# Kernel optimization log

Hardware: AMD Instinct MI355X
Metric: run time of the kernel (lower is better)

The kernel has to match this reference:

```python
import jax, jax.numpy as jnp
import numpy as np

N = 65536      # total nodes
B = 128        # graphs per batch
NPG = N // B   # nodes per graph (equal-size graphs)
IN = 128       # in_channels
H = 128        # hidden_channels
E = 1048576    # spatial edges
K = 8          # kNN neighbors
L = 3          # num_layers
EPS = 1e-5     # GraphNorm eps
SLOPE = 0.01   # leaky_relu default negative_slope


def setup_inputs() -> dict:
    key = jax.random.key(0)
    ks = jax.random.split(key, 16)
    x = jax.random.normal(ks[0], (N, IN), jnp.float32)
    edge_index = jax.random.randint(ks[1], (2, E), 0, N, dtype=jnp.int32)
    batch = jnp.repeat(jnp.arange(B, dtype=jnp.int32), NPG)
    s = 0.05
    inp = {
        'x': x, 'edge_index': edge_index, 'batch': batch,
        'emb_w': jax.random.normal(ks[2], (IN, H), jnp.float32) * s,
        'emb_b': jax.random.normal(ks[3], (H,), jnp.float32) * s,
        'conv_w': jax.random.normal(ks[4], (L - 1, H, H), jnp.float32) * s,
        'conv_b': jax.random.normal(ks[5], (L - 1, H), jnp.float32) * s,
        'fconv_w': jax.random.normal(ks[6], (L - 1, H, H), jnp.float32) * s,
        'fconv_b': jax.random.normal(ks[7], (L - 1, H), jnp.float32) * s,
        'norm_w': 1.0 + jax.random.normal(ks[8], (L - 1, H), jnp.float32) * s,
        'norm_b': jax.random.normal(ks[9], (L - 1, H), jnp.float32) * s,
        'norm_ms': 1.0 + jax.random.normal(ks[10], (L - 1, H), jnp.float32) * s,
        'fnorm_w': 1.0 + jax.random.normal(ks[11], (L - 1, H), jnp.float32) * s,
        'fnorm_b': jax.random.normal(ks[12], (L - 1, H), jnp.float32) * s,
        'fnorm_ms': 1.0 + jax.random.normal(ks[13], (L - 1, H), jnp.float32) * s,
    }
    return inp


def _segment_mean(v, seg, num):
    s = jax.ops.segment_sum(v, seg, num_segments=num)
    c = jax.ops.segment_sum(jnp.ones((v.shape[0], 1), v.dtype), seg, num_segments=num)
    return s / jnp.maximum(c, 1.0)


def _gcn_conv(h, src, dst, W, b):
    # GCNConv: h @ W, add self-loops, symmetric normalization, scatter-add.
    hw = h @ W
    deg = jax.ops.segment_sum(jnp.ones(src.shape[0], hw.dtype), dst, num_segments=N) + 1.0
    dinv = jax.lax.rsqrt(deg)
    msgs = (dinv[src] * dinv[dst])[:, None] * hw[src]
    agg = jnp.zeros_like(hw).at[dst].add(msgs)
    agg = agg + (dinv * dinv)[:, None] * hw  # self-loop contribution
    return agg + b


def _graph_norm(v, batch, w, bsh, ms):
    mean = _segment_mean(v, batch, B)                  # [B,H]
    out = v - mean[batch] * ms
    var = _segment_mean(out * out, batch, B)
    std = jnp.sqrt(var + EPS)
    return w * out / std[batch] + bsh


def _knn_graph_cosine(h):
    # per-graph cosine kNN (loop=False); equal-size graphs -> blocked [B,n,n] sim
    hb = h.reshape(B, NPG, H)
    nrm = jnp.linalg.norm(hb, axis=-1, keepdims=True)
    hn = hb / jnp.maximum(nrm, 1e-12)
    sim = jnp.einsum('bnd,bmd->bnm', hn, hn)
    sim = sim - 2.0 * jnp.eye(NPG, dtype=sim.dtype)    # exclude self-loops
    _, idx = jax.lax.top_k(sim, K)                     # [B,NPG,K] in-graph ids
    offs = (jnp.arange(B, dtype=idx.dtype) * NPG)[:, None, None]
    src = (idx + offs).reshape(-1).astype(jnp.int32)   # neighbors (sources)
    dst = jnp.repeat(jnp.arange(N, dtype=jnp.int32), K)
    return src, dst


def reference(x, edge_index, batch, emb_w, emb_b, conv_w, conv_b, fconv_w, fconv_b,
              norm_w, norm_b, norm_ms, fnorm_w, fnorm_b, fnorm_ms):
    h = x @ emb_w + emb_b
    fsrc, fdst = _knn_graph_cosine(h)
    src, dst = edge_index[0], edge_index[1]
    all_h = []
    for i in range(L - 1):
        h1 = _gcn_conv(h, src, dst, conv_w[i], conv_b[i])
        h1 = _graph_norm(h1, batch, norm_w[i], norm_b[i], norm_ms[i])
        h1 = jax.nn.leaky_relu(h1, SLOPE)              # dropout is identity (eval)
        f = _gcn_conv(h1, fsrc, fdst, fconv_w[i], fconv_b[i])
        f = _graph_norm(f, batch, fnorm_w[i], fnorm_b[i], fnorm_ms[i])
        f = jax.nn.leaky_relu(f, SLOPE)
        h = (h1 + f) * 0.5
        all_h.append(h)
    # faithful to original: indexes all_x[i-1] for i in range(num_layers)
    gf = jnp.zeros((B, H), h.dtype)
    for i in range(L):
        gf = gf + _segment_mean(all_h[i - 1], batch, B)
    return gf
```

## Files before the change

### kernel.cpp

```cpp
#include <hip/hip_runtime.h>

typedef unsigned short u16;
typedef unsigned int   u32;
typedef unsigned char  u8;
typedef __bf16 bf16x8 __attribute__((ext_vector_type(8)));
typedef unsigned short us8 __attribute__((ext_vector_type(8)));
typedef float f32x4 __attribute__((ext_vector_type(4)));

#define NN 65536
#define EE 1048576
#define NPGC 512
#define BGR 128
#define EMAX 32
#define NB 128
#define BSLOT 96
#define EBSLOT 10240
#define FP8S 32.0f
#define FP8SI (1.0f/32.0f)

__device__ inline float bf2f(u16 b){ u32 u=((u32)b)<<16; float f; __builtin_memcpy(&f,&u,4); return f; }
__device__ inline u16 f2bf(float f){ u32 u; __builtin_memcpy(&u,&f,4); u32 r=(u+0x7FFFu+((u>>16)&1u))>>16; return (u16)r; }
__device__ inline u8 f2fp8(float f){
  int p = __builtin_amdgcn_cvt_pk_fp8_f32(f, f, 0, false);
  return (u8)(p & 0xFF);
}

struct PTab { const void* src[9]; int off[9]; };
__global__ __launch_bounds__(256) void prep_params(const float* __restrict__ emb_w,
    const float* __restrict__ conv_w, const float* __restrict__ fconv_w, u16* __restrict__ pwt,
    PTab tab, u16* __restrict__ pw)
{
  int i = blockIdx.x*256 + threadIdx.x;
  if (i < 5*16384) {
    int m = i >> 14, j = i & 16383;
    int n = j >> 7, k = j & 127;
    const float* src = (m == 0) ? emb_w : (m <= 2) ? conv_w + (m-1)*16384 : fconv_w + (m-3)*16384;
    pwt[i] = f2bf(src[k*128 + n]);
  } else {
    int s = i - 5*16384;
    if (s < 2176) {
      int t = 0;
      #pragma unroll
      for (int k = 1; k < 9; k++) if (s >= tab.off[k]) t = k;
      pw[s] = f2bf(((const float*)tab.src[t])[s - tab.off[t]]);
    }
  }
}

__global__ __launch_bounds__(256) void bucket_edges(const int* __restrict__ srcp,
    const int* __restrict__ dstp, int* __restrict__ boff, u32* __restrict__ ebuf)
{
  __shared__ u32 buf[NB][BSLOT];
  __shared__ int cnt[NB], gbase[NB];
  const int tid = threadIdx.x;
  for (int b = tid; b < NB; b += 256) cnt[b] = 0;
  __syncthreads();
  const int base = blockIdx.x * 4096;
  #pragma unroll
  for (int v = 0; v < 4; v++) {
    const int e = base + (v*256 + tid)*4;
    int4 dv = *reinterpret_cast<const int4*>(dstp + e);
    int4 sv = *reinterpret_cast<const int4*>(srcp + e);
    #pragma unroll
    for (int t = 0; t < 4; t++) {
      u32 d = ((u32)((&dv.x)[t])) & (NN-1);
      u32 s = ((u32)((&sv.x)[t])) & (NN-1);
      int b = d >> 9;
      int p = atomicAdd(&cnt[b], 1);
      if (p < BSLOT) buf[b][p] = (d << 16) | s;
    }
  }
  __syncthreads();
  for (int b = tid; b < NB; b += 256) gbase[b] = atomicAdd(&boff[b], min(cnt[b], BSLOT));
  __syncthreads();
  const int wave = tid >> 6, lane = tid & 63;
  for (int b = wave; b < NB; b += 4) {
    const int c = min(cnt[b], BSLOT);
    const int gb = gbase[b];
    for (int i = lane; i < c; i += 64) {
      int gi = gb + i;
      if (gi < EBSLOT) ebuf[(size_t)b*EBSLOT + gi] = buf[b][i];
    }
  }
}

__global__ __launch_bounds__(256) void fill_ell(const int* __restrict__ boff,
    const u32* __restrict__ ebuf, int* __restrict__ pos, u16* __restrict__ elln)
{
  __shared__ u16 lell[512*EMAX];
  __shared__ int lcnt[512];
  const int b = blockIdx.x;
  const int tid = threadIdx.x;
  for (int i = tid; i < 512; i += 256) lcnt[i] = 0;
  __syncthreads();
  const int cnt = min(boff[b], EBSLOT);
  const u32* eb = ebuf + (size_t)b*EBSLOT;
  for (int i = tid; i < cnt; i += 256) {
    u32 v = eb[i];
    int dl = (v >> 16) & 511;
    int p = atomicAdd(&lcnt[dl], 1);
    if (p < EMAX) lell[dl*EMAX + p] = (u16)(v & 0xFFFFu);
  }
  __syncthreads();
  const int nbase = b * 512;
  for (int i = tid; i < 512; i += 256) pos[nbase + i] = lcnt[i];
  u32* dst = reinterpret_cast<u32*>(elln + ((size_t)nbase << 5));
  const u32* src = reinterpret_cast<const u32*>(lell);
  for (int i = tid; i < 512*16; i += 256) dst[i] = src[i];
}

__global__ __launch_bounds__(256) void gemm_emb_bt(const float* __restrict__ X,
    const u16* __restrict__ BtE, const u16* __restrict__ bias, const u16* __restrict__ BtC,
    const int* __restrict__ pos, u16* __restrict__ Ch, float* __restrict__ rinv,
    u8* __restrict__ Chw)
{
  __shared__ __align__(16) u16 hs[64][136];
  const int tid = threadIdx.x;
  const int wave = tid >> 6, lane = tid & 63, q = lane >> 4, l15 = lane & 15;
  const long arow = (long)blockIdx.x*64 + wave*16 + l15;
  const float* Ap = X + arow*128;
  f32x4 acc[8] = {};
  #pragma unroll
  for (int ks = 0; ks < 4; ks++) {
    const int k0 = ks*32 + q*8;
    float4 u0 = *reinterpret_cast<const float4*>(Ap + k0);
    float4 u1 = *reinterpret_cast<const float4*>(Ap + k0 + 4);
    us8 a;
    a[0]=f2bf(u0.x); a[1]=f2bf(u0.y); a[2]=f2bf(u0.z); a[3]=f2bf(u0.w);
    a[4]=f2bf(u1.x); a[5]=f2bf(u1.y); a[6]=f2bf(u1.z); a[7]=f2bf(u1.w);
    bf16x8 af = __builtin_bit_cast(bf16x8, a);
    #pragma unroll
    for (int nt = 0; nt < 8; nt++) {
      bf16x8 bf = __builtin_bit_cast(bf16x8,
          *reinterpret_cast<const us8*>(BtE + (nt*16 + l15)*128 + k0));
      acc[nt] = __builtin_amdgcn_mfma_f32_16x16x32_bf16(af, bf, acc[nt], 0, 0, 0);
    }
  }
  const long orow0 = (long)blockIdx.x*64 + wave*16 + q*4;
  float bvt[8];
  #pragma unroll
  for (int nt = 0; nt < 8; nt++) bvt[nt] = bf2f(bias[nt*16 + l15]);
  #pragma unroll
  for (int r = 0; r < 4; r++) {
    float ss = 0.f;
    const int lrow = wave*16 + q*4 + r;
    #pragma unroll
    for (int nt = 0; nt < 8; nt++) {
      float hv = acc[nt][r] + bvt[nt];
      u16 hb = f2bf(hv);
      Ch[(orow0 + r)*128 + nt*16 + l15] = hb;
      hs[lrow][nt*16 + l15] = hb;
      ss += hv*hv;
    }
    #pragma unroll
    for (int m = 1; m < 16; m <<= 1) ss += __shfl_xor(ss, m, 64);
    if (l15 == 0) rinv[orow0 + r] = 1.0f / fmaxf(sqrtf(ss), 1e-12f);
  }
  f32x4 acc2[8] = {};
  #pragma unroll
  for (int ks = 0; ks < 4; ks++) {
    const int k0 = ks*32 + q*8;
    bf16x8 af = __builtin_bit_cast(bf16x8,
        *reinterpret_cast<const us8*>(&hs[wave*16 + l15][k0]));
    #pragma unroll
    for (int nt = 0; nt < 8; nt++) {
      bf16x8 bf = __builtin_bit_cast(bf16x8,
          *reinterpret_cast<const us8*>(BtC + (nt*16 + l15)*128 + k0));
      acc2[nt] = __builtin_amdgcn_mfma_f32_16x16x32_bf16(af, bf, acc2[nt], 0, 0, 0);
    }
  }
  float scl[4];
  #pragma unroll
  for (int r = 0; r < 4; r++) scl[r] = rsqrtf((float)pos[orow0 + r] + 1.0f) * FP8S;
  #pragma unroll
  for (int nt = 0; nt < 8; nt++) {
    int col = nt*16 + l15;
    #pragma unroll
    for (int r = 0; r < 4; r++)
      Chw[(orow0 + r)*128 + col] = f2fp8(acc2[nt][r] * scl[r]);
  }
}

__global__ __launch_bounds__(256) void gemm_norm(const u16* __restrict__ h1raw,
    const u16* __restrict__ Bt, const float* __restrict__ ssum, const float* __restrict__ ssq,
    const u16* __restrict__ gw, const u16* __restrict__ gb, const u16* __restrict__ gms,
    u16* __restrict__ h1norm, u16* __restrict__ C)
{
  __shared__ float As[4][128], Bs[4][128];
  const int tid = threadIdx.x;
  const int gidx = blockIdx.x >> 3;
  const int wave = tid >> 6, lane = tid & 63, q = lane >> 4, l15 = lane & 15;
  #pragma unroll
  for (int cc = 0; cc < 2; cc++) {
    int c = cc*64 + lane;
    float mean = ssum[gidx*128 + c] * (1.0f/512.0f);
    float e2   = ssq [gidx*128 + c] * (1.0f/512.0f);
    float sub  = mean * bf2f(gms[c]);
    float var  = e2 - 2.0f*sub*mean + sub*sub;
    float istd = rsqrtf(var + 1e-5f);
    float A = istd * bf2f(gw[c]);
    As[wave][c] = A;
    Bs[wave][c] = bf2f(gb[c]) - sub*A;
  }
  const long arow = (long)blockIdx.x*64 + wave*16 + l15;
  const u16* Ap = h1raw + arow*128;
  f32x4 acc[8] = {};
  #pragma unroll
  for (int ks = 0; ks < 4; ks++) {
    const int k0 = ks*32 + q*8;
    us8 raw = *reinterpret_cast<const us8*>(Ap + k0);
    us8 af;
    #pragma unroll
    for (int j = 0; j < 8; j++) {
      float o = As[wave][k0+j] * bf2f(raw[j]) + Bs[wave][k0+j];
      o = (o >= 0.f) ? o : 0.01f * o;
      af[j] = f2bf(o);
    }
    *reinterpret_cast<us8*>(h1norm + arow*128 + k0) = af;
    bf16x8 afv = __builtin_bit_cast(bf16x8, af);
    #pragma unroll
    for (int nt = 0; nt < 8; nt++) {
      bf16x8 bf = __builtin_bit_cast(bf16x8,
          *reinterpret_cast<const us8*>(Bt + (nt*16 + l15)*128 + k0));
      acc[nt] = __builtin_amdgcn_mfma_f32_16x16x32_bf16(afv, bf, acc[nt], 0, 0, 0);
    }
  }
  const long orow0 = (long)blockIdx.x*64 + wave*16 + q*4;
  #pragma unroll
  for (int nt = 0; nt < 8; nt++) {
    int col = nt*16 + l15;
    #pragma unroll
    for (int r = 0; r < 4; r++)
      C[(orow0 + r)*128 + col] = f2bf(acc[nt][r]);
  }
}

__global__ __launch_bounds__(256) void gn_apply_gemm(const u16* __restrict__ fraw,
    const u16* __restrict__ h1n, const u16* __restrict__ Bt,
    const float* __restrict__ ssum, const float* __restrict__ ssq,
    const u16* __restrict__ gw, const u16* __restrict__ gb, const u16* __restrict__ gms,
    const int* __restrict__ pos, float* __restrict__ gf, u8* __restrict__ C)
{
  __shared__ float As[4][128], Bs[4][128];
  __shared__ float gpart[4][128];
  const int tid = threadIdx.x;
  const int gidx = blockIdx.x >> 3;
  const int wave = tid >> 6, lane = tid & 63, q = lane >> 4, l15 = lane & 15;
  #pragma unroll
  for (int cc = 0; cc < 2; cc++) {
    int c = cc*64 + lane;
    float mean = ssum[gidx*128 + c] * (1.0f/512.0f);
    float e2   = ssq [gidx*128 + c] * (1.0f/512.0f);
    float sub  = mean * bf2f(gms[c]);
    float var  = e2 - 2.0f*sub*mean + sub*sub;
    float istd = rsqrtf(var + 1e-5f);
    float A = istd * bf2f(gw[c]);
    As[wave][c] = A;
    Bs[wave][c] = bf2f(gb[c]) - sub*A;
  }
  const long arow = (long)blockIdx.x*64 + wave*16 + l15;
  const u16* Fp = fraw + arow*128;
  const u16* Hp = h1n  + arow*128;
  f32x4 acc[8] = {};
  float hv[4][8];
  #pragma unroll
  for (int ks = 0; ks < 4; ks++) {
    const int k0 = ks*32 + q*8;
    us8 fr = *reinterpret_cast<const us8*>(Fp + k0);
    us8 hr = *reinterpret_cast<const us8*>(Hp + k0);
    us8 af;
    #pragma unroll
    for (int j = 0; j < 8; j++) {
      float o = As[wave][k0+j] * bf2f(fr[j]) + Bs[wave][k0+j];
      o = (o >= 0.f) ? o : 0.01f * o;
      float h = 0.5f * (bf2f(hr[j]) + o);
      hv[ks][j] = h;
      af[j] = f2bf(h);
    }
    bf16x8 afv = __builtin_bit_cast(bf16x8, af);
    #pragma unroll
    for (int nt = 0; nt < 8; nt++) {
      bf16x8 bf = __builtin_bit_cast(bf16x8,
          *reinterpret_cast<const us8*>(Bt + (nt*16 + l15)*128 + k0));
      acc[nt] = __builtin_amdgcn_mfma_f32_16x16x32_bf16(afv, bf, acc[nt], 0, 0, 0);
    }
  }
  const long orow0 = (long)blockIdx.x*64 + wave*16 + q*4;
  float scl[4];
  #pragma unroll
  for (int r = 0; r < 4; r++) scl[r] = rsqrtf((float)pos[orow0 + r] + 1.0f) * FP8S;
  #pragma unroll
  for (int nt = 0; nt < 8; nt++) {
    int col = nt*16 + l15;
    #pragma unroll
    for (int r = 0; r < 4; r++)
      C[(orow0 + r)*128 + col] = f2fp8(acc[nt][r] * scl[r]);
  }
  #pragma unroll
  for (int ks = 0; ks < 4; ks++) {
    #pragma unroll
    for (int j = 0; j < 8; j++) {
      float v = hv[ks][j];
      v += __shfl_xor(v, 1, 64);
      v += __shfl_xor(v, 2, 64);
      v += __shfl_xor(v, 4, 64);
      v += __shfl_xor(v, 8, 64);
      if (l15 == 0) gpart[wave][ks*32 + q*8 + j] = v;
    }
  }
  __syncthreads();
  if (tid < 128) {
    float s = gpart[0][tid] + gpart[1][tid] + gpart[2][tid] + gpart[3][tid];
    atomicAdd(&gf[gidx*128 + tid], s * (1.0f/512.0f));
  }
}

__device__ inline u32 mkkey(float v, u32 col){
  u32 b; __builtin_memcpy(&b, &v, 4);
  b ^= (u32)(((int)b >> 31)) | 0x80000000u;
  return (b & 0xFFFFFE00u) | col;
}
#define TOP8_INS(tv, key) { \
  tv[0] = max(tv[0], (key)); \
  u32 lo_, hi_; \
  lo_ = min(tv[0],tv[1]); hi_ = max(tv[0],tv[1]); tv[0]=lo_; tv[1]=hi_; \
  lo_ = min(tv[1],tv[2]); hi_ = max(tv[1],tv[2]); tv[1]=lo_; tv[2]=hi_; \
  lo_ = min(tv[2],tv[3]); hi_ = max(tv[2],tv[3]); tv[2]=lo_; tv[3]=hi_; \
  lo_ = min(tv[3],tv[4]); hi_ = max(tv[3],tv[4]); tv[3]=lo_; tv[4]=hi_; \
  lo_ = min(tv[4],tv[5]); hi_ = max(tv[4],tv[5]); tv[4]=lo_; tv[5]=hi_; \
  lo_ = min(tv[5],tv[6]); hi_ = max(tv[5],tv[6]); tv[5]=lo_; tv[6]=hi_; \
  lo_ = min(tv[6],tv[7]); hi_ = max(tv[6],tv[7]); tv[6]=lo_; tv[7]=hi_; }

__global__ __launch_bounds__(256, 4) void knn_topk(const u16* __restrict__ h,
    const float* __restrict__ rinv, int* __restrict__ fsrc)
{
  __shared__ __align__(16) u16 Bb[64*136];
  __shared__ __align__(16) u32 simb[64*68];
  __shared__ float rb[64];
  const int tid = threadIdx.x;
  const int g = blockIdx.x & 127, tile = blockIdx.x >> 7;
  const int gbase = g * NPGC;
  const int abase = gbase + tile * 64;
  const int wave = tid >> 6, lane = tid & 63, q = lane >> 4, l15 = lane & 15;

  us8 afr[4];
  #pragma unroll
  for (int ks = 0; ks < 4; ks++)
    afr[ks] = *reinterpret_cast<const us8*>(h + (size_t)(abase + wave*16 + l15)*128 + ks*32 + q*8);

  const int r0 = tid >> 4, c80 = (tid & 15) * 8;
  us8 breg[4];
  #pragma unroll
  for (int it = 0; it < 4; it++)
    breg[it] = *reinterpret_cast<const us8*>(h + (size_t)(gbase + r0 + it*16)*128 + c80);
  float rbreg = (tid < 64) ? rinv[gbase + tid] : 0.f;

  const int srow = tid >> 2, ssub = tid & 3;
  u32 tv[8];
  #pragma unroll
  for (int t = 0; t < 8; t++) tv[t] = 0u;

  for (int ch = 0; ch < 8; ch++) {
    #pragma unroll
    for (int it = 0; it < 4; it++)
      *reinterpret_cast<us8*>(&Bb[(r0 + it*16)*136 + c80]) = breg[it];
    if (tid < 64) rb[tid] = rbreg;
    __syncthreads();
    if (ch < 7) {
      #pragma unroll
      for (int it = 0; it < 4; it++)
        breg[it] = *reinterpret_cast<const us8*>(h + (size_t)(gbase + (ch+1)*64 + r0 + it*16)*128 + c80);
      if (tid < 64) rbreg = rinv[gbase + (ch+1)*64 + tid];
    }
    f32x4 acc[4] = {};
    #pragma unroll
    for (int ks = 0; ks < 4; ks++) {
      int k0 = ks*32 + q*8;
      bf16x8 af = __builtin_bit_cast(bf16x8, afr[ks]);
      #pragma unroll
      for (int ct = 0; ct < 4; ct++) {
        bf16x8 bf = __builtin_bit_cast(bf16x8, *reinterpret_cast<const us8*>(&Bb[(ct*16 + l15)*136 + k0]));
        acc[ct] = __builtin_amdgcn_mfma_f32_16x16x32_bf16(af, bf, acc[ct], 0, 0, 0);
      }
    }
    #pragma unroll
    for (int ct = 0; ct < 4; ct++) {
      int lc = ct*16 + l15;
      float rbv = rb[lc];
      #pragma unroll
      for (int r = 0; r < 4; r++) {
        int lr = wave*16 + q*4 + r;
        u32 key = mkkey(acc[ct][r] * rbv, (u32)(ch*64 + lc));
        if (tile*64 + lr == ch*64 + lc) key = 0u;
        simb[lr*68 + lc] = key;
      }
    }
    __syncthreads();
    const u32* sp = &simb[srow*68 + ssub*16];
    #pragma unroll
    for (int u = 0; u < 4; u++) {
      uint4 kv = *reinterpret_cast<const uint4*>(sp + 4*u);
      TOP8_INS(tv, kv.x); TOP8_INS(tv, kv.y); TOP8_INS(tv, kv.z); TOP8_INS(tv, kv.w);
    }
    __syncthreads();
  }
  u32* candk = simb;
  #pragma unroll
  for (int t = 0; t < 8; t++) candk[srow*33 + ssub*8 + t] = tv[t];
  __syncthreads();
  if (tid < 64) {
    u32 bv[8];
    #pragma unroll
    for (int t = 0; t < 8; t++) bv[t] = 0u;
    for (int t = 0; t < 32; t++) {
      u32 key = candk[tid*33 + t];
      TOP8_INS(bv, key);
    }
    size_t node = abase + tid;
    #pragma unroll
    for (int k2 = 0; k2 < 8; k2++) fsrc[node*8 + k2] = gbase + (int)(bv[k2] & 511u);
  }
}

__device__ inline void acc4(u32 vv, bool on, float& a0, float& a1, float& a2, float& a3){
  float c0 = __builtin_amdgcn_cvt_f32_fp8((int)vv, 0);
  float c1 = __builtin_amdgcn_cvt_f32_fp8((int)vv, 1);
  float c2 = __builtin_amdgcn_cvt_f32_fp8((int)vv, 2);
  float c3 = __builtin_amdgcn_cvt_f32_fp8((int)vv, 3);
  a0 += on ? c0 : 0.f; a1 += on ? c1 : 0.f;
  a2 += on ? c2 : 0.f; a3 += on ? c3 : 0.f;
}
__global__ __launch_bounds__(256) void agg_spatial(const u32* __restrict__ hw32,
    const u16* __restrict__ elln, const int* __restrict__ pos,
    const u16* __restrict__ bias, u16* __restrict__ outp,
    float* __restrict__ ssum, float* __restrict__ ssq)
{
  __shared__ f32x4 sred[4][64], qred[4][64];
  const int g = blockIdx.x & 127, sub = blockIdx.x >> 7;
  const int wave = threadIdx.x >> 6, lane = threadIdx.x & 63;
  const int half = lane >> 5, cl = lane & 31;
  const int nbase = g*NPGC + sub*32 + wave*8;
  float bv[4];
  #pragma unroll
  for (int k = 0; k < 4; k++) bv[k] = bf2f(bias[4*cl + k]);
  float sa0=0,sa1=0,sa2=0,sa3=0, qa0=0,qa1=0,qa2=0,qa3=0;
  for (int t = 0; t < 4; t++) {
    const int node = nbase + 2*t + half;
    const u16* row = elln + ((size_t)node << 5);
    const int tot = pos[node];
    const int d = min(tot, EMAX);
    const int dmax = max(d, __shfl_xor(d, 32, 64));
    const float dnS = rsqrtf((float)tot + 1.0f) * FP8SI;
    const u32 sv = hw32[(size_t)node*32 + cl];
    float a0=0,a1=0,a2=0,a3=0;
    if (dmax > 0) {
      us8 iv0 = *reinterpret_cast<const us8*>(row);
      us8 iv1 = *reinterpret_cast<const us8*>(row + 8);
      u32 v[16];
      #pragma unroll
      for (int u = 0; u < 8; u++) v[u] = hw32[(size_t)iv0[u]*32 + cl];
      const bool two = (dmax > 8);
      if (two) {
        #pragma unroll
        for (int u = 0; u < 8; u++) v[8+u] = hw32[(size_t)iv1[u]*32 + cl];
      }
      #pragma unroll
      for (int u = 0; u < 8; u++) acc4(v[u], u < d, a0, a1, a2, a3);
      if (two) {
        #pragma unroll
        for (int u = 0; u < 8; u++) acc4(v[8+u], 8+u < d, a0, a1, a2, a3);
      }
    }
    if (dmax > 16) {
      us8 iv2 = *reinterpret_cast<const us8*>(row + 16);
      us8 iv3 = *reinterpret_cast<const us8*>(row + 24);
      u32 v[16];
      #pragma unroll
      for (int u = 0; u < 8; u++) v[u] = hw32[(size_t)iv2[u]*32 + cl];
      const bool four = (dmax > 24);
      if (four) {
        #pragma unroll
        for (int u = 0; u < 8; u++) v[8+u] = hw32[(size_t)iv3[u]*32 + cl];
      }
      #pragma unroll
      for (int u = 0; u < 8; u++) acc4(v[u], 16+u < d, a0, a1, a2, a3);
      if (four) {
        #pragma unroll
        for (int u = 0; u < 8; u++) acc4(v[8+u], 24+u < d, a0, a1, a2, a3);
      }
    }
    acc4(sv, true, a0, a1, a2, a3);
    float r0 = dnS*a0 + bv[0], r1 = dnS*a1 + bv[1];
    float r2 = dnS*a2 + bv[2], r3 = dnS*a3 + bv[3];
    u32* op = reinterpret_cast<u32*>(outp) + (size_t)node*64 + 2*cl;
    op[0] = (u32)f2bf(r0) | ((u32)f2bf(r1) << 16);
    op[1] = (u32)f2bf(r2) | ((u32)f2bf(r3) << 16);
    sa0 += r0; sa1 += r1; sa2 += r2; sa3 += r3;
    qa0 += r0*r0; qa1 += r1*r1; qa2 += r2*r2; qa3 += r3*r3;
  }
  sred[wave][lane] = (f32x4){sa0, sa1, sa2, sa3};
  qred[wave][lane] = (f32x4){qa0, qa1, qa2, qa3};
  __syncthreads();
  const int tid = threadIdx.x;
  if (tid < 128) {
    const int ccl = tid >> 2, k = tid & 3;
    float s = 0.f, qq = 0.f;
    #pragma unroll
    for (int w = 0; w < 4; w++) {
      s  += sred[w][ccl][k] + sred[w][32+ccl][k];
      qq += qred[w][ccl][k] + qred[w][32+ccl][k];
    }
    atomicAdd(&ssum[g*128 + tid], s);
    atomicAdd(&ssq [g*128 + tid], qq);
  }
}

__global__ __launch_bounds__(256) void agg_knn(const u16* __restrict__ hw, const int* __restrict__ fsrc,
    const u16* __restrict__ bias, u16* __restrict__ outp,
    float* __restrict__ ssum, float* __restrict__ ssq)
{
  __shared__ float4 red[4][64];
  const int g = blockIdx.x & 127, sub = blockIdx.x >> 7;
  const int wave = threadIdx.x >> 6, lane = threadIdx.x & 63;
  const int nbase = g*NPGC + sub*32 + wave*8;
  const u32* hwp = reinterpret_cast<const u32*>(hw);
  const float bv0 = bf2f(bias[2*lane]), bv1 = bf2f(bias[2*lane+1]);
  const float c = 1.0f / 9.0f;
  float s0 = 0.f, s1 = 0.f, q0 = 0.f, q1 = 0.f;
  for (int t = 0; t < 8; t++) {
    const int node = nbase + t;
    const int* fr = fsrc + (long)node*8;
    u32 sv = hwp[(long)node*64 + lane];
    float a0 = bf2f((u16)sv), a1 = bf2f((u16)(sv>>16));
    #pragma unroll
    for (int k2 = 0; k2 < 8; k2++) {
      int s = fr[k2] & (NN-1);
      u32 v = hwp[(long)s*64 + lane];
      a0 += bf2f((u16)v); a1 += bf2f((u16)(v>>16));
    }
    float r0 = a0*c + bv0;
    float r1 = a1*c + bv1;
    reinterpret_cast<u32*>(outp)[(long)node*64 + lane] = (u32)f2bf(r0) | ((u32)f2bf(r1) << 16);
    s0 += r0; s1 += r1; q0 += r0*r0; q1 += r1*r1;
  }
  red[wave][lane] = make_float4(s0, s1, q0, q1);
  __syncthreads();
  if (wave == 0) {
    float4 a = red[0][lane];
    #pragma unroll
    for (int k = 1; k < 4; k++) {
      float4 b = red[k][lane];
      a.x += b.x; a.y += b.y; a.z += b.z; a.w += b.w;
    }
    atomicAdd(&ssum[g*128 + 2*lane],     a.x);
    atomicAdd(&ssum[g*128 + 2*lane + 1], a.y);
    atomicAdd(&ssq [g*128 + 2*lane],     a.z);
    atomicAdd(&ssq [g*128 + 2*lane + 1], a.w);
  }
}

__global__ __launch_bounds__(1024) void gn_final(const u16* __restrict__ v, const u16* __restrict__ h1n,
    const float* __restrict__ ssum, const float* __restrict__ ssq,
    const u16* __restrict__ gw, const u16* __restrict__ gb, const u16* __restrict__ gms,
    const float* __restrict__ gf, float* __restrict__ outf)
{
  __shared__ float red[1024];
  const int tid = threadIdx.x;
  const int g = blockIdx.x >> 1, half = blockIdx.x & 1;
  const int cl = tid & 63, c = half*64 + cl;
  const int rsub = tid >> 6;
  const long base = (long)g * NPGC * 128;
  float mean = ssum[g*128 + c] * (1.0f/512.0f);
  float e2   = ssq [g*128 + c] * (1.0f/512.0f);
  float sub  = mean * bf2f(gms[c]);
  float var  = e2 - 2.0f*sub*mean + sub*sub;
  float istd = rsqrtf(var + 1e-5f);
  float A = istd * bf2f(gw[c]);
  float B = bf2f(gb[c]) - sub*A;
  float gsum = 0.f;
  for (int r = rsub; r < NPGC; r += 16) {
    long idx = base + (long)r*128 + c;
    float o = A * bf2f(v[idx]) + B;
    o = (o >= 0.f) ? o : 0.01f * o;
    o = 0.5f * (bf2f(h1n[idx]) + o);
    gsum += o;
  }
  red[tid] = gsum; __syncthreads();
  if (tid < 64) {
    float t = 0.f;
    for (int k = 0; k < 16; k++) t += red[cl + k*64];
    int oi = g*128 + half*64 + tid;
    outf[oi] = gf[oi] + 2.0f * t * (1.0f/512.0f);
  }
}

extern "C" void kernel_launch(void* const* d_in, const int* in_sizes, int n_in,
                              void* d_out, int out_size, void* d_ws, size_t ws_size,
                              hipStream_t stream)
{
  const float* x  = (const float*)d_in[0];
  const int*   ei = (const int*)d_in[1];

  char* p = (char*)d_ws;
  auto alloc = [&](size_t b){ void* r = (void*)p; p += ((b + 255) & ~(size_t)255); return r; };
  u16*   h_bf   = (u16*)  alloc((size_t)NN*128*2);
  u16*   f_bf   = (u16*)  alloc((size_t)NN*128*2);
  u16*   h1_bf  = (u16*)  alloc((size_t)NN*128*2);
  int*   fsrc   = (int*)  alloc((size_t)NN*8*4);
  u16*   elln   = (u16*)  alloc((size_t)NN*32*2);
  float* rinv   = (float*)alloc((size_t)NN*4);
  u32*   ebuf   = (u32*)  alloc((size_t)NB*EBSLOT*4);
  int*   pos    = (int*)  alloc((size_t)NN*4);
  int*   boff   = (int*)  alloc((size_t)NB*4);
  float* gf     = (float*)alloc((size_t)BGR*128*4);
  float* stats  = (float*)alloc((size_t)8*BGR*128*4);
  u16*   pw     = (u16*)  alloc((size_t)2176*2);
  u16*   pwt    = (u16*)  alloc((size_t)5*16384*2);
  char*  shared = (char*) alloc((size_t)NN*128*2);
  u16*   hw_bf   = (u16*)shared;
  u8*    hw_f8   = (u8*) shared;

  const int O_EMBB=0, O_CONVB=128, O_FCONVB=384, O_NW=640, O_NB2=896, O_NMS=1152,
            O_FNW=1408, O_FNB=1664, O_FNMS=1920;
  PTab tab;
  const int srcidx[9] = {4,6,8,9,10,11,12,13,14};
  const int offs[9]   = {O_EMBB,O_CONVB,O_FCONVB,O_NW,O_NB2,O_NMS,O_FNW,O_FNB,O_FNMS};
  for (int t = 0; t < 9; t++) { tab.src[t] = d_in[srcidx[t]]; tab.off[t] = offs[t]; }

  const int* srcp = ei;
  const int* dstp = ei + EE;

  (void)hipMemsetAsync(boff, 0,
      (size_t)NB*4 + 256 - (size_t)NB*4 + (size_t)BGR*128*4 + (size_t)8*BGR*128*4, stream);

  prep_params<<<329, 256, 0, stream>>>((const float*)d_in[3], (const float*)d_in[5],
                                       (const float*)d_in[7], pwt, tab, pw);
  bucket_edges<<<256, 256, 0, stream>>>(srcp, dstp, boff, ebuf);
  fill_ell<<<128, 256, 0, stream>>>(boff, ebuf, pos, elln);
  gemm_emb_bt<<<1024, 256, 0, stream>>>(x, pwt + 0, pw + O_EMBB, pwt + 1*16384, pos,
                                        h_bf, rinv, hw_f8);
  knn_topk<<<1024, 256, 0, stream>>>(h_bf, rinv, fsrc);

  float* ssS0 = stats + 0*BGR*128; float* sqS0 = stats + 1*BGR*128;
  float* ssF0 = stats + 2*BGR*128; float* sqF0 = stats + 3*BGR*128;
  float* ssS1 = stats + 4*BGR*128; float* sqS1 = stats + 5*BGR*128;
  float* ssF1 = stats + 6*BGR*128; float* sqF1 = stats + 7*BGR*128;

  agg_spatial<<<2048, 256, 0, stream>>>((const u32*)hw_f8, elln, pos, pw + O_CONVB,
                                        h1_bf, ssS0, sqS0);
  gemm_norm<<<1024, 256, 0, stream>>>(h1_bf, pwt + 3*16384, ssS0, sqS0,
                                      pw + O_NW, pw + O_NB2, pw + O_NMS,
                                      h_bf , hw_bf);
  agg_knn<<<2048, 256, 0, stream>>>(hw_bf, fsrc, pw + O_FCONVB, f_bf, ssF0, sqF0);
  gn_apply_gemm<<<1024, 256, 0, stream>>>(f_bf, h_bf, pwt + 2*16384, ssF0, sqF0,
                                          pw + O_FNW, pw + O_FNB, pw + O_FNMS,
                                          pos, gf, hw_f8);
  agg_spatial<<<2048, 256, 0, stream>>>((const u32*)hw_f8, elln, pos, pw + O_CONVB + 128,
                                        h1_bf, ssS1, sqS1);
  gemm_norm<<<1024, 256, 0, stream>>>(h1_bf, pwt + 4*16384, ssS1, sqS1,
                                      pw + O_NW + 128, pw + O_NB2 + 128, pw + O_NMS + 128,
                                      h_bf , hw_bf);
  agg_knn<<<2048, 256, 0, stream>>>(hw_bf, fsrc, pw + O_FCONVB + 128, f_bf, ssF1, sqF1);
  gn_final<<<256, 1024, 0, stream>>>(f_bf, h_bf, ssF1, sqF1,
                                     pw + O_FNW + 128, pw + O_FNB + 128, pw + O_FNMS + 128,
                                     gf, (float*)d_out);
}
```

Before: 385.9 us.

## Split GEMM kernels' output columns across wave pairs, doubling grid size

```diff
diff --git a/kernel.cpp b/kernel.cpp
--- a/kernel.cpp
+++ b/kernel.cpp
@@ -114,12 +114,14 @@
     const int* __restrict__ pos, u16* __restrict__ Ch, float* __restrict__ rinv,
     u8* __restrict__ Chw)
 {
-  __shared__ __align__(16) u16 hs[64][136];
+  __shared__ __align__(16) u16 hs[32][136];
+  __shared__ float rpart[2][32];
   const int tid = threadIdx.x;
   const int wave = tid >> 6, lane = tid & 63, q = lane >> 4, l15 = lane & 15;
-  const long arow = (long)blockIdx.x*64 + wave*16 + l15;
+  const int rt = wave >> 1, ch2 = wave & 1;
+  const long arow = (long)blockIdx.x*32 + rt*16 + l15;
   const float* Ap = X + arow*128;
-  f32x4 acc[8] = {};
+  f32x4 acc[4] = {};
   #pragma unroll
   for (int ks = 0; ks < 4; ks++) {
     const int k0 = ks*32 + q*8;
@@ -130,42 +132,47 @@
     a[4]=f2bf(u1.x); a[5]=f2bf(u1.y); a[6]=f2bf(u1.z); a[7]=f2bf(u1.w);
     bf16x8 af = __builtin_bit_cast(bf16x8, a);
     #pragma unroll
-    for (int nt = 0; nt < 8; nt++) {
+    for (int nt = 0; nt < 4; nt++) {
       bf16x8 bf = __builtin_bit_cast(bf16x8,
-          *reinterpret_cast<const us8*>(BtE + (nt*16 + l15)*128 + k0));
+          *reinterpret_cast<const us8*>(BtE + (ch2*64 + nt*16 + l15)*128 + k0));
       acc[nt] = __builtin_amdgcn_mfma_f32_16x16x32_bf16(af, bf, acc[nt], 0, 0, 0);
     }
   }
-  const long orow0 = (long)blockIdx.x*64 + wave*16 + q*4;
-  float bvt[8];
-  #pragma unroll
-  for (int nt = 0; nt < 8; nt++) bvt[nt] = bf2f(bias[nt*16 + l15]);
+  const long orow0 = (long)blockIdx.x*32 + rt*16 + q*4;
+  float bvt[4];
+  #pragma unroll
+  for (int nt = 0; nt < 4; nt++) bvt[nt] = bf2f(bias[ch2*64 + nt*16 + l15]);
   #pragma unroll
   for (int r = 0; r < 4; r++) {
     float ss = 0.f;
-    const int lrow = wave*16 + q*4 + r;
-    #pragma unroll
-    for (int nt = 0; nt < 8; nt++) {
+    const int lrow = rt*16 + q*4 + r;
+    #pragma unroll
+    for (int nt = 0; nt < 4; nt++) {
       float hv = acc[nt][r] + bvt[nt];
       u16 hb = f2bf(hv);
-      Ch[(orow0 + r)*128 + nt*16 + l15] = hb;
-      hs[lrow][nt*16 + l15] = hb;
+      Ch[(orow0 + r)*128 + ch2*64 + nt*16 + l15] = hb;
+      hs[lrow][ch2*64 + nt*16 + l15] = hb;
       ss += hv*hv;
     }
     #pragma unroll
     for (int m = 1; m < 16; m <<= 1) ss += __shfl_xor(ss, m, 64);
-    if (l15 == 0) rinv[orow0 + r] = 1.0f / fmaxf(sqrtf(ss), 1e-12f);
-  }
-  f32x4 acc2[8] = {};
+    if (l15 == 0) rpart[ch2][lrow] = ss;
+  }
+  __syncthreads();
+  if (tid < 32) {
+    float ss = rpart[0][tid] + rpart[1][tid];
+    rinv[(long)blockIdx.x*32 + tid] = 1.0f / fmaxf(sqrtf(ss), 1e-12f);
+  }
+  f32x4 acc2[4] = {};
   #pragma unroll
   for (int ks = 0; ks < 4; ks++) {
     const int k0 = ks*32 + q*8;
     bf16x8 af = __builtin_bit_cast(bf16x8,
-        *reinterpret_cast<const us8*>(&hs[wave*16 + l15][k0]));
-    #pragma unroll
-    for (int nt = 0; nt < 8; nt++) {
+        *reinterpret_cast<const us8*>(&hs[rt*16 + l15][k0]));
+    #pragma unroll
+    for (int nt = 0; nt < 4; nt++) {
       bf16x8 bf = __builtin_bit_cast(bf16x8,
-          *reinterpret_cast<const us8*>(BtC + (nt*16 + l15)*128 + k0));
+          *reinterpret_cast<const us8*>(BtC + (ch2*64 + nt*16 + l15)*128 + k0));
       acc2[nt] = __builtin_amdgcn_mfma_f32_16x16x32_bf16(af, bf, acc2[nt], 0, 0, 0);
     }
   }
@@ -173,8 +180,8 @@
   #pragma unroll
   for (int r = 0; r < 4; r++) scl[r] = rsqrtf((float)pos[orow0 + r] + 1.0f) * FP8S;
   #pragma unroll
-  for (int nt = 0; nt < 8; nt++) {
-    int col = nt*16 + l15;
+  for (int nt = 0; nt < 4; nt++) {
+    int col = ch2*64 + nt*16 + l15;
     #pragma unroll
     for (int r = 0; r < 4; r++)
       Chw[(orow0 + r)*128 + col] = f2fp8(acc2[nt][r] * scl[r]);
@@ -188,8 +195,9 @@
 {
   __shared__ float As[4][128], Bs[4][128];
   const int tid = threadIdx.x;
-  const int gidx = blockIdx.x >> 3;
+  const int gidx = blockIdx.x >> 4;
   const int wave = tid >> 6, lane = tid & 63, q = lane >> 4, l15 = lane & 15;
+  const int rt = wave >> 1, ch2 = wave & 1;
   #pragma unroll
   for (int cc = 0; cc < 2; cc++) {
     int c = cc*64 + lane;
@@ -202,9 +210,9 @@
     As[wave][c] = A;
     Bs[wave][c] = bf2f(gb[c]) - sub*A;
   }
-  const long arow = (long)blockIdx.x*64 + wave*16 + l15;
+  const long arow = (long)blockIdx.x*32 + rt*16 + l15;
   const u16* Ap = h1raw + arow*128;
-  f32x4 acc[8] = {};
+  f32x4 acc[4] = {};
   #pragma unroll
   for (int ks = 0; ks < 4; ks++) {
     const int k0 = ks*32 + q*8;
@@ -216,19 +224,20 @@
       o = (o >= 0.f) ? o : 0.01f * o;
       af[j] = f2bf(o);
     }
-    *reinterpret_cast<us8*>(h1norm + arow*128 + k0) = af;
+    if (ch2 == 0)
+      *reinterpret_cast<us8*>(h1norm + arow*128 + k0) = af;
     bf16x8 afv = __builtin_bit_cast(bf16x8, af);
     #pragma unroll
-    for (int nt = 0; nt < 8; nt++) {
+    for (int nt = 0; nt < 4; nt++) {
       bf16x8 bf = __builtin_bit_cast(bf16x8,
-          *reinterpret_cast<const us8*>(Bt + (nt*16 + l15)*128 + k0));
+          *reinterpret_cast<const us8*>(Bt + (ch2*64 + nt*16 + l15)*128 + k0));
       acc[nt] = __builtin_amdgcn_mfma_f32_16x16x32_bf16(afv, bf, acc[nt], 0, 0, 0);
     }
   }
-  const long orow0 = (long)blockIdx.x*64 + wave*16 + q*4;
-  #pragma unroll
-  for (int nt = 0; nt < 8; nt++) {
-    int col = nt*16 + l15;
+  const long orow0 = (long)blockIdx.x*32 + rt*16 + q*4;
+  #pragma unroll
+  for (int nt = 0; nt < 4; nt++) {
+    int col = ch2*64 + nt*16 + l15;
     #pragma unroll
     for (int r = 0; r < 4; r++)
       C[(orow0 + r)*128 + col] = f2bf(acc[nt][r]);
@@ -242,10 +251,11 @@
     const int* __restrict__ pos, float* __restrict__ gf, u8* __restrict__ C)
 {
   __shared__ float As[4][128], Bs[4][128];
-  __shared__ float gpart[4][128];
-  const int tid = threadIdx.x;
-  const int gidx = blockIdx.x >> 3;
+  __shared__ float gpart[2][128];
+  const int tid = threadIdx.x;
+  const int gidx = blockIdx.x >> 4;
   const int wave = tid >> 6, lane = tid & 63, q = lane >> 4, l15 = lane & 15;
+  const int rt = wave >> 1, ch2 = wave & 1;
   #pragma unroll
   for (int cc = 0; cc < 2; cc++) {
     int c = cc*64 + lane;
@@ -258,10 +268,10 @@
     As[wave][c] = A;
     Bs[wave][c] = bf2f(gb[c]) - sub*A;
   }
-  const long arow = (long)blockIdx.x*64 + wave*16 + l15;
+  const long arow = (long)blockIdx.x*32 + rt*16 + l15;
   const u16* Fp = fraw + arow*128;
   const u16* Hp = h1n  + arow*128;
-  f32x4 acc[8] = {};
+  f32x4 acc[4] = {};
   float hv[4][8];
   #pragma unroll
   for (int ks = 0; ks < 4; ks++) {
@@ -279,19 +289,19 @@
     }
     bf16x8 afv = __builtin_bit_cast(bf16x8, af);
     #pragma unroll
-    for (int nt = 0; nt < 8; nt++) {
+    for (int nt = 0; nt < 4; nt++) {
       bf16x8 bf = __builtin_bit_cast(bf16x8,
-          *reinterpret_cast<const us8*>(Bt + (nt*16 + l15)*128 + k0));
+          *reinterpret_cast<const us8*>(Bt + (ch2*64 + nt*16 + l15)*128 + k0));
       acc[nt] = __builtin_amdgcn_mfma_f32_16x16x32_bf16(afv, bf, acc[nt], 0, 0, 0);
     }
   }
-  const long orow0 = (long)blockIdx.x*64 + wave*16 + q*4;
+  const long orow0 = (long)blockIdx.x*32 + rt*16 + q*4;
   float scl[4];
   #pragma unroll
   for (int r = 0; r < 4; r++) scl[r] = rsqrtf((float)pos[orow0 + r] + 1.0f) * FP8S;
   #pragma unroll
-  for (int nt = 0; nt < 8; nt++) {
-    int col = nt*16 + l15;
+  for (int nt = 0; nt < 4; nt++) {
+    int col = ch2*64 + nt*16 + l15;
     #pragma unroll
     for (int r = 0; r < 4; r++)
       C[(orow0 + r)*128 + col] = f2fp8(acc[nt][r] * scl[r]);
@@ -305,12 +315,12 @@
       v += __shfl_xor(v, 2, 64);
       v += __shfl_xor(v, 4, 64);
       v += __shfl_xor(v, 8, 64);
-      if (l15 == 0) gpart[wave][ks*32 + q*8 + j] = v;
+      if (l15 == 0 && ch2 == 0) gpart[rt][ks*32 + q*8 + j] = v;
     }
   }
   __syncthreads();
   if (tid < 128) {
-    float s = gpart[0][tid] + gpart[1][tid] + gpart[2][tid] + gpart[3][tid];
+    float s = gpart[0][tid] + gpart[1][tid];
     atomicAdd(&gf[gidx*128 + tid], s * (1.0f/512.0f));
   }
 }
@@ -631,13 +641,13 @@
   const int* dstp = ei + EE;
 
   (void)hipMemsetAsync(boff, 0,
-      (size_t)NB*4 + 256 - (size_t)NB*4 + (size_t)BGR*128*4 + (size_t)8*BGR*128*4, stream);
+      (size_t)256 + (size_t)BGR*128*4 + (size_t)8*BGR*128*4, stream);
 
   prep_params<<<329, 256, 0, stream>>>((const float*)d_in[3], (const float*)d_in[5],
                                        (const float*)d_in[7], pwt, tab, pw);
   bucket_edges<<<256, 256, 0, stream>>>(srcp, dstp, boff, ebuf);
   fill_ell<<<128, 256, 0, stream>>>(boff, ebuf, pos, elln);
-  gemm_emb_bt<<<1024, 256, 0, stream>>>(x, pwt + 0, pw + O_EMBB, pwt + 1*16384, pos,
+  gemm_emb_bt<<<2048, 256, 0, stream>>>(x, pwt + 0, pw + O_EMBB, pwt + 1*16384, pos,
                                         h_bf, rinv, hw_f8);
   knn_topk<<<1024, 256, 0, stream>>>(h_bf, rinv, fsrc);
 
@@ -648,16 +658,16 @@
 
   agg_spatial<<<2048, 256, 0, stream>>>((const u32*)hw_f8, elln, pos, pw + O_CONVB,
                                         h1_bf, ssS0, sqS0);
-  gemm_norm<<<1024, 256, 0, stream>>>(h1_bf, pwt + 3*16384, ssS0, sqS0,
+  gemm_norm<<<2048, 256, 0, stream>>>(h1_bf, pwt + 3*16384, ssS0, sqS0,
                                       pw + O_NW, pw + O_NB2, pw + O_NMS,
                                       h_bf , hw_bf);
   agg_knn<<<2048, 256, 0, stream>>>(hw_bf, fsrc, pw + O_FCONVB, f_bf, ssF0, sqF0);
-  gn_apply_gemm<<<1024, 256, 0, stream>>>(f_bf, h_bf, pwt + 2*16384, ssF0, sqF0,
+  gn_apply_gemm<<<2048, 256, 0, stream>>>(f_bf, h_bf, pwt + 2*16384, ssF0, sqF0,
                                           pw + O_FNW, pw + O_FNB, pw + O_FNMS,
                                           pos, gf, hw_f8);
   agg_spatial<<<2048, 256, 0, stream>>>((const u32*)hw_f8, elln, pos, pw + O_CONVB + 128,
                                         h1_bf, ssS1, sqS1);
-  gemm_norm<<<1024, 256, 0, stream>>>(h1_bf, pwt + 4*16384, ssS1, sqS1,
+  gemm_norm<<<2048, 256, 0, stream>>>(h1_bf, pwt + 4*16384, ssS1, sqS1,
                                       pw + O_NW + 128, pw + O_NB2 + 128, pw + O_NMS + 128,
                                       h_bf , hw_bf);
   agg_knn<<<2048, 256, 0, stream>>>(hw_bf, fsrc, pw + O_FCONVB + 128, f_bf, ssF1, sqF1);
```

New measurement: 394.1 us. 1.02x slower.
